# Performance work log

Hardware: AMD Instinct MI355X
Metric: run time of the kernel (lower is better)

The kernel has to match this reference:

```python
import jax, jax.numpy as jnp
import numpy as np

N_C, N_E, IN_FEAT, OUT_FEAT = 8192, 8192, 256, 128


def setup_inputs() -> dict:
    key = jax.random.key(0)
    ks = jax.random.split(key, 9)
    s = 1.0 / np.sqrt(IN_FEAT)
    return {
        "emb_cause": jax.random.normal(ks[0], (N_C, IN_FEAT), jnp.float32),
        "emb_effect": jax.random.normal(ks[1], (N_E, IN_FEAT), jnp.float32),
        "causal_mask": jax.random.randint(ks[2], (N_C, N_E), 0, 2, jnp.int32),
        "Wq": jax.random.uniform(ks[3], (IN_FEAT, OUT_FEAT), jnp.float32, -s, s),
        "bq": jax.random.uniform(ks[4], (OUT_FEAT,), jnp.float32, -s, s),
        "Wk": jax.random.uniform(ks[5], (IN_FEAT, OUT_FEAT), jnp.float32, -s, s),
        "bk": jax.random.uniform(ks[6], (OUT_FEAT,), jnp.float32, -s, s),
        "Wv": jax.random.uniform(ks[7], (IN_FEAT, OUT_FEAT), jnp.float32, -s, s),
        "bv": jax.random.uniform(ks[8], (OUT_FEAT,), jnp.float32, -s, s),
    }


def reference(emb_cause, emb_effect, causal_mask, Wq, bq, Wk, bk, Wv, bv):
    Q = emb_cause @ Wq + bq          # [N_c, D]
    K = emb_effect @ Wk + bk         # [N_e, D]
    V = emb_effect @ Wv + bv         # [N_e, D]
    scale = 1.0 / jnp.sqrt(jnp.asarray(Q.shape[-1], Q.dtype))
    scores = (Q @ K.T) * scale       # [N_c, N_e]
    scores = jnp.where(causal_mask == 0, -jnp.inf, scores)
    attn_weights = jax.nn.softmax(scores, axis=-1)
    causal_output = attn_weights @ V  # [N_c, D]
    return causal_output, attn_weights
```

## Files before the change

### kernel.cpp

```cpp
#include <hip/hip_runtime.h>

#define NC   8192
#define NEFF 8192
#define DIN  256
#define DOUT 128
#define SCALE 0.08838834764831843f

typedef float  f32x4  __attribute__((ext_vector_type(4)));
typedef short  s16x8  __attribute__((ext_vector_type(8)));
typedef short  s16x4  __attribute__((ext_vector_type(4)));
typedef unsigned long long u64;

__device__ __forceinline__ short f2bf(float f) {
    unsigned int u = __builtin_bit_cast(unsigned int, f);
    u += 0x7FFFu + ((u >> 16) & 1u);
    return (short)(u >> 16);
}

__device__ __forceinline__ s16x8 ld8(const short* p) {
    return *(const s16x8*)__builtin_assume_aligned(p, 16);
}

__device__ __forceinline__ unsigned getdw(int4 v, int i) {
    switch (i & 3) {
        case 0: return (unsigned)v.x;
        case 1: return (unsigned)v.y;
        case 2: return (unsigned)v.z;
        default: return (unsigned)v.w;
    }
}


__global__ __launch_bounds__(256) void pack_kernel(
    const int* __restrict__ mask, u64* __restrict__ bm)
{
    const size_t stride = (size_t)gridDim.x * 256;
    const size_t i0 = (size_t)blockIdx.x * 256 + threadIdx.x;
    const bool lead = (threadIdx.x & 63) == 0;
    for (size_t i = i0; i < (size_t)NC * NEFF; i += 8 * stride) {
        int m[8];
#pragma unroll
        for (int j = 0; j < 8; j++) m[j] = mask[i + j * stride];
        u64 b[8];
#pragma unroll
        for (int j = 0; j < 8; j++) b[j] = __ballot(m[j] != 0);
        if (lead) {
#pragma unroll
            for (int j = 0; j < 8; j++) bm[(i + j * stride) >> 6] = b[j];
        }
    }
}

__global__ __launch_bounds__(256, 2) void qkv_kernel(
    const float* __restrict__ embc, const float* __restrict__ embe,
    const float* __restrict__ Wq, const float* __restrict__ bq,
    const float* __restrict__ Wk, const float* __restrict__ bk,
    const float* __restrict__ Wv, const float* __restrict__ bv,
    short* __restrict__ Qf, short* __restrict__ Kf, short* __restrict__ Vf)
{
    const int mat = blockIdx.y;
    const float* src  = (mat == 0) ? embc : embe;
    const float* W    = (mat == 0) ? Wq : (mat == 1 ? Wk : Wv);
    const float* bias = (mat == 0) ? bq : (mat == 1 ? bk : bv);

    __shared__ short wt[DOUT][136];
    __shared__ short tbuf[4][16][132];
    __shared__ short tbufV[128][68];

    const int tid  = threadIdx.x;
    const int wave = tid >> 6, lane = tid & 63;
    const int quad = lane >> 4, ln16 = lane & 15;
    const int rowbase = blockIdx.x * 64;
    const int arow = rowbase + wave * 16 + ln16;

    f32x4 acc[8];
#pragma unroll
    for (int i = 0; i < 8; i++) acc[i] = (f32x4){0.f, 0.f, 0.f, 0.f};

    for (int h = 0; h < 2; h++) {
        __syncthreads();
        {
            const int n0 = (tid & 31) * 4;
            const int kb = tid >> 5;
#pragma unroll
            for (int i = 0; i < 16; i++) {
                const int k = kb + i * 8;
                const float4 w4 = *(const float4*)(W + (size_t)(h * 128 + k) * DOUT + n0);
                wt[n0 + 0][k] = f2bf(w4.x);
                wt[n0 + 1][k] = f2bf(w4.y);
                wt[n0 + 2][k] = f2bf(w4.z);
                wt[n0 + 3][k] = f2bf(w4.w);
            }
        }
        __syncthreads();

        s16x8 afr[4];
#pragma unroll
        for (int kc = 0; kc < 4; kc++) {
            const float* ap = src + (size_t)arow * DIN + h * 128 + kc * 32 + quad * 8;
            const float4 a0 = *(const float4*)ap;
            const float4 a1 = *(const float4*)(ap + 4);
            s16x8 a;
            a[0] = f2bf(a0.x); a[1] = f2bf(a0.y); a[2] = f2bf(a0.z); a[3] = f2bf(a0.w);
            a[4] = f2bf(a1.x); a[5] = f2bf(a1.y); a[6] = f2bf(a1.z); a[7] = f2bf(a1.w);
            afr[kc] = a;
        }
#pragma unroll
        for (int nt = 0; nt < 8; nt++) {
#pragma unroll
            for (int kc = 0; kc < 4; kc++) {
                const s16x8 b = ld8(&wt[nt * 16 + ln16][kc * 32 + quad * 8]);
                acc[nt] = __builtin_amdgcn_mfma_f32_16x16x32_bf16(afr[kc], b, acc[nt], 0, 0, 0);
            }
        }
    }

    if (mat < 2) {
        short* dst = (mat == 0) ? Qf : Kf;
        const float sc = (mat == 0) ? SCALE : 1.0f;
#pragma unroll
        for (int nt = 0; nt < 8; nt++) {
            const float bb = bias[nt * 16 + ln16];
#pragma unroll
            for (int r = 0; r < 4; r++)
                tbuf[wave][quad * 4 + r][nt * 16 + ln16] = f2bf((acc[nt][r] + bb) * sc);
        }
        const int tile = blockIdx.x * 4 + wave;
#pragma unroll
        for (int kc = 0; kc < 4; kc++) {
            const s16x8 fr = ld8(&tbuf[wave][ln16][kc * 32 + quad * 8]);
            *(s16x8*)(dst + ((size_t)(tile * 4 + kc) * 64 + lane) * 8) = fr;
        }
    } else {
#pragma unroll
        for (int nt = 0; nt < 8; nt++) {
            const float bb = bias[nt * 16 + ln16];
#pragma unroll
            for (int r = 0; r < 4; r++)
                tbufV[nt * 16 + ln16][wave * 16 + quad * 4 + r] = f2bf(acc[nt][r] + bb);
        }
        __syncthreads();
        const int ct = blockIdx.x >> 1;
        const int ksub0 = (blockIdx.x & 1) * 2;
        const int ks = wave & 1;
#pragma unroll
        for (int t = 0; t < 4; t++) {
            const int nt2 = (wave >> 1) * 4 + t;
            const s16x8 fr = ld8(&tbufV[nt2 * 16 + ln16][ks * 32 + quad * 8]);
            *(s16x8*)(Vf + ((size_t)((ct * 8 + nt2) * 4 + ksub0 + ks) * 64 + lane) * 8) = fr;
        }
    }
}

__global__ __launch_bounds__(256, 5) void stats_kernel(
    const unsigned int* __restrict__ bm, const short* __restrict__ Qf,
    const short* __restrict__ Kf, float* __restrict__ lsum)
{
    const int bx = blockIdx.x, strip = blockIdx.y;
    const int tid  = threadIdx.x;
    const int wave = tid >> 6, lane = tid & 63;
    const int quad = lane >> 4, ln16 = lane & 15;
    const int rowbase = bx * 128 + wave * 32;
    const int t0 = rowbase >> 4;

    s16x8 aq[2][4];
#pragma unroll
    for (int rs = 0; rs < 2; rs++)
#pragma unroll
        for (int kc = 0; kc < 4; kc++)
            aq[rs][kc] = ld8(Qf + ((size_t)((t0 + rs) * 4 + kc) * 64 + lane) * 8);

    float lp[2] = {0.f, 0.f};

    for (int it = 0; it < 2; it++) {
        const int cb = strip * 256 + it * 128;

        int4 bmv[2];
#pragma unroll
        for (int rs = 0; rs < 2; rs++)
            bmv[rs] = *(const int4*)(bm + (size_t)(rowbase + rs * 16 + ln16) * 256 + (cb >> 5));

#pragma unroll
        for (int nt = 0; nt < 8; nt++) {
            s16x8 bq[4];
#pragma unroll
            for (int kc = 0; kc < 4; kc++)
                bq[kc] = ld8(Kf + ((size_t)(((cb >> 4) + nt) * 4 + kc) * 64 + lane) * 8);
            f32x4 c0 = (f32x4){0.f, 0.f, 0.f, 0.f};
            f32x4 c1 = (f32x4){0.f, 0.f, 0.f, 0.f};
#pragma unroll
            for (int kc = 0; kc < 4; kc++) {
                c0 = __builtin_amdgcn_mfma_f32_16x16x32_bf16(bq[kc], aq[0][kc], c0, 0, 0, 0);
                c1 = __builtin_amdgcn_mfma_f32_16x16x32_bf16(bq[kc], aq[1][kc], c1, 0, 0, 0);
            }
#pragma unroll
            for (int rs = 0; rs < 2; rs++) {
                const unsigned d = getdw(bmv[rs], nt >> 1);
#pragma unroll
                for (int r = 0; r < 4; r++) {
                    const float cv = rs ? c1[r] : c0[r];
                    if ((d >> ((nt & 1) * 16 + quad * 4 + r)) & 1u)
                        lp[rs] += __expf(cv);
                }
            }
        }
    }

#pragma unroll
    for (int rs = 0; rs < 2; rs++) {
        float v = lp[rs];
        v += __shfl_xor(v, 16);
        v += __shfl_xor(v, 32);
        if (quad == 0)
            atomicAdd(&lsum[rowbase + rs * 16 + ln16], v);
    }
}

__global__ __launch_bounds__(256, 3) void attn_kernel(
    const short* __restrict__ Qf, const short* __restrict__ Kf,
    const short* __restrict__ Vf, const float* __restrict__ lsum,
    const unsigned int* __restrict__ bm,
    float* __restrict__ outO, float* __restrict__ outW)
{
    __shared__ short wlds[4][32][132];

    const int bx = blockIdx.x, strip = blockIdx.y;
    const int tid  = threadIdx.x;
    const int wave = tid >> 6, lane = tid & 63;
    const int quad = lane >> 4, ln16 = lane & 15;
    const int rowbase = bx * 128 + wave * 32;
    const int t0 = rowbase >> 4;

    s16x8 aq[2][4];
#pragma unroll
    for (int rs = 0; rs < 2; rs++)
#pragma unroll
        for (int kc = 0; kc < 4; kc++)
            aq[rs][kc] = ld8(Qf + ((size_t)((t0 + rs) * 4 + kc) * 64 + lane) * 8);

    float rl[2];
#pragma unroll
    for (int rs = 0; rs < 2; rs++)
        rl[rs] = 1.0f / lsum[rowbase + rs * 16 + ln16];

    f32x4 o[2][8];
#pragma unroll
    for (int rs = 0; rs < 2; rs++)
#pragma unroll
        for (int i = 0; i < 8; i++) o[rs][i] = (f32x4){0.f, 0.f, 0.f, 0.f};

    for (int it = 0; it < 2; it++) {
        const int cb = strip * 256 + it * 128;

        int4 bmv[2];
#pragma unroll
        for (int rs = 0; rs < 2; rs++)
            bmv[rs] = *(const int4*)(bm + (size_t)(rowbase + rs * 16 + ln16) * 256 + (cb >> 5));

#pragma unroll
        for (int nt = 0; nt < 8; nt++) {
            s16x8 bq[4];
#pragma unroll
            for (int kc = 0; kc < 4; kc++)
                bq[kc] = ld8(Kf + ((size_t)(((cb >> 4) + nt) * 4 + kc) * 64 + lane) * 8);
            f32x4 c0 = (f32x4){0.f, 0.f, 0.f, 0.f};
            f32x4 c1 = (f32x4){0.f, 0.f, 0.f, 0.f};
#pragma unroll
            for (int kc = 0; kc < 4; kc++) {
                c0 = __builtin_amdgcn_mfma_f32_16x16x32_bf16(bq[kc], aq[0][kc], c0, 0, 0, 0);
                c1 = __builtin_amdgcn_mfma_f32_16x16x32_bf16(bq[kc], aq[1][kc], c1, 0, 0, 0);
            }
#pragma unroll
            for (int rs = 0; rs < 2; rs++) {
                const unsigned d = getdw(bmv[rs], nt >> 1);
                float wv[4];
#pragma unroll
                for (int r = 0; r < 4; r++) {
                    const float cv = rs ? c1[r] : c0[r];
                    wv[r] = ((d >> ((nt & 1) * 16 + quad * 4 + r)) & 1u)
                                ? __expf(cv) * rl[rs] : 0.0f;
                }
                const int row = rowbase + rs * 16 + ln16;
                float4 w4; w4.x = wv[0]; w4.y = wv[1]; w4.z = wv[2]; w4.w = wv[3];
                *(float4*)(outW + (size_t)row * NEFF + cb + nt * 16 + quad * 4) = w4;
                s16x4 p4;
                p4[0] = f2bf(wv[0]); p4[1] = f2bf(wv[1]);
                p4[2] = f2bf(wv[2]); p4[3] = f2bf(wv[3]);
                *(s16x4*)__builtin_assume_aligned(
                    &wlds[wave][rs * 16 + ln16][nt * 16 + quad * 4], 8) = p4;
            }
        }

#pragma unroll
        for (int ks = 0; ks < 4; ks++) {
            const s16x8 aw0 = ld8(&wlds[wave][ln16][ks * 32 + quad * 8]);
            const s16x8 aw1 = ld8(&wlds[wave][16 + ln16][ks * 32 + quad * 8]);
#pragma unroll
            for (int nt2 = 0; nt2 < 8; nt2++) {
                const s16x8 bv = ld8(Vf + ((size_t)(((cb >> 7) * 8 + nt2) * 4 + ks) * 64 + lane) * 8);
                o[0][nt2] = __builtin_amdgcn_mfma_f32_16x16x32_bf16(aw0, bv, o[0][nt2], 0, 0, 0);
                o[1][nt2] = __builtin_amdgcn_mfma_f32_16x16x32_bf16(aw1, bv, o[1][nt2], 0, 0, 0);
            }
        }
    }

#pragma unroll
    for (int rs = 0; rs < 2; rs++)
#pragma unroll
        for (int nt2 = 0; nt2 < 8; nt2++)
#pragma unroll
            for (int r = 0; r < 4; r++) {
                const int row = rowbase + rs * 16 + quad * 4 + r;
                atomicAdd(&outO[(size_t)row * DOUT + nt2 * 16 + ln16], o[rs][nt2][r]);
            }
}

extern "C" void kernel_launch(void* const* d_in, const int* in_sizes, int n_in,
                              void* d_out, int out_size, void* d_ws, size_t ws_size,
                              hipStream_t stream) {
    (void)in_sizes; (void)n_in; (void)out_size; (void)ws_size;

    const float* embc = (const float*)d_in[0];
    const float* embe = (const float*)d_in[1];
    const int*   mask = (const int*)d_in[2];
    const float* Wq = (const float*)d_in[3];
    const float* bq = (const float*)d_in[4];
    const float* Wk = (const float*)d_in[5];
    const float* bk = (const float*)d_in[6];
    const float* Wv = (const float*)d_in[7];
    const float* bv = (const float*)d_in[8];

    char* ws = (char*)d_ws;
    short* Qf = (short*)(ws);
    short* Kf = (short*)(ws + (2u << 20));
    short* Vf = (short*)(ws + (4u << 20));
    float* lsum = (float*)(ws + (6u << 20));
    unsigned int* bm = (unsigned int*)(ws + (8u << 20));

    float* outO = (float*)d_out;
    float* outW = outO + (size_t)NC * DOUT;

    hipMemsetAsync(lsum, 0, NC * sizeof(float), stream);
    hipMemsetAsync(outO, 0, (size_t)NC * DOUT * sizeof(float), stream);

    pack_kernel<<<8192, 256, 0, stream>>>(mask, (u64*)bm);
    qkv_kernel<<<dim3(128, 3), 256, 0, stream>>>(embc, embe, Wq, bq, Wk, bk, Wv, bv,
                                                 Qf, Kf, Vf);
    stats_kernel<<<dim3(64, 32), 256, 0, stream>>>(bm, Qf, Kf, lsum);
    attn_kernel<<<dim3(64, 32), 256, 0, stream>>>(Qf, Kf, Vf, lsum, bm, outO, outW);
}
```

Measured before the change: 679.2 us.

## Transpose stats MFMA output layout and halve stats grid with wider strips

The stats kernel now swaps the MFMA operands so each lane holds scores for four rows at one column. The mask bits are then indexed by ln16, and the row sums are reduced across 16 lanes instead of across quads. Each block now covers 512 columns instead of 256, so the grid has half as many strips, fewer atomics are issued, and the loaded Q fragments are reused more. The cost is more registers (8 accumulators and 8 mask vectors), which the occupancy hint lowers from 5 to 4, plus more reduction shuffles.

```diff
diff --git a/kernel.cpp b/kernel.cpp
--- a/kernel.cpp
+++ b/kernel.cpp
@@ -152,7 +152,7 @@
     }
 }
 
-__global__ __launch_bounds__(256, 5) void stats_kernel(
+__global__ __launch_bounds__(256, 4) void stats_kernel(
     const unsigned int* __restrict__ bm, const short* __restrict__ Qf,
     const short* __restrict__ Kf, float* __restrict__ lsum)
 {
@@ -170,15 +170,17 @@
         for (int kc = 0; kc < 4; kc++)
             aq[rs][kc] = ld8(Qf + ((size_t)((t0 + rs) * 4 + kc) * 64 + lane) * 8);
 
-    float lp[2] = {0.f, 0.f};
-
-    for (int it = 0; it < 2; it++) {
-        const int cb = strip * 256 + it * 128;
-
-        int4 bmv[2];
+    float lp[8] = {0.f, 0.f, 0.f, 0.f, 0.f, 0.f, 0.f, 0.f};
+
+    for (int it = 0; it < 4; it++) {
+        const int cb = strip * 512 + it * 128;
+
+        int4 bmv[2][4];
 #pragma unroll
         for (int rs = 0; rs < 2; rs++)
-            bmv[rs] = *(const int4*)(bm + (size_t)(rowbase + rs * 16 + ln16) * 256 + (cb >> 5));
+#pragma unroll
+            for (int r = 0; r < 4; r++)
+                bmv[rs][r] = *(const int4*)(bm + (size_t)(rowbase + rs * 16 + quad * 4 + r) * 256 + (cb >> 5));
 
 #pragma unroll
         for (int nt = 0; nt < 8; nt++) {
@@ -190,29 +192,28 @@
             f32x4 c1 = (f32x4){0.f, 0.f, 0.f, 0.f};
 #pragma unroll
             for (int kc = 0; kc < 4; kc++) {
-                c0 = __builtin_amdgcn_mfma_f32_16x16x32_bf16(bq[kc], aq[0][kc], c0, 0, 0, 0);
-                c1 = __builtin_amdgcn_mfma_f32_16x16x32_bf16(bq[kc], aq[1][kc], c1, 0, 0, 0);
-            }
-#pragma unroll
-            for (int rs = 0; rs < 2; rs++) {
-                const unsigned d = getdw(bmv[rs], nt >> 1);
+                c0 = __builtin_amdgcn_mfma_f32_16x16x32_bf16(aq[0][kc], bq[kc], c0, 0, 0, 0);
+                c1 = __builtin_amdgcn_mfma_f32_16x16x32_bf16(aq[1][kc], bq[kc], c1, 0, 0, 0);
+            }
+#pragma unroll
+            for (int rs = 0; rs < 2; rs++)
 #pragma unroll
                 for (int r = 0; r < 4; r++) {
+                    const unsigned d = getdw(bmv[rs][r], nt >> 1);
                     const float cv = rs ? c1[r] : c0[r];
-                    if ((d >> ((nt & 1) * 16 + quad * 4 + r)) & 1u)
-                        lp[rs] += __expf(cv);
+                    if ((d >> ((nt & 1) * 16 + ln16)) & 1u)
+                        lp[rs * 4 + r] += __expf(cv);
                 }
-            }
-        }
-    }
-
-#pragma unroll
-    for (int rs = 0; rs < 2; rs++) {
-        float v = lp[rs];
-        v += __shfl_xor(v, 16);
-        v += __shfl_xor(v, 32);
-        if (quad == 0)
-            atomicAdd(&lsum[rowbase + rs * 16 + ln16], v);
+        }
+    }
+
+#pragma unroll
+    for (int i = 0; i < 8; i++) {
+        float v = lp[i];
+        v += __shfl_xor(v, 1); v += __shfl_xor(v, 2);
+        v += __shfl_xor(v, 4); v += __shfl_xor(v, 8);
+        if (ln16 == 0)
+            atomicAdd(&lsum[rowbase + (i >> 2) * 16 + quad * 4 + (i & 3)], v);
     }
 }
 
@@ -346,6 +347,6 @@
     pack_kernel<<<8192, 256, 0, stream>>>(mask, (u64*)bm);
     qkv_kernel<<<dim3(128, 3), 256, 0, stream>>>(embc, embe, Wq, bq, Wk, bk, Wv, bv,
                                                  Qf, Kf, Vf);
-    stats_kernel<<<dim3(64, 32), 256, 0, stream>>>(bm, Qf, Kf, lsum);
+    stats_kernel<<<dim3(64, 16), 256, 0, stream>>>(bm, Qf, Kf, lsum);
     attn_kernel<<<dim3(64, 32), 256, 0, stream>>>(Qf, Kf, Vf, lsum, bm, outO, outW);
 }
```

After: 685.6 us. No clear change (+0.9%).

## Retile attention kernel to 16 rows per wave and longer column strips

Applied to the files above, without the earlier changes.

The attention kernel now gives each wave 16 query rows instead of 32 and walks 1024 columns per block instead of 256. The grid changes to 128x8 and launch bounds are raised for occupancy. Fewer strips per row means fewer atomicAdd partial sums into the output. The cost is that each K/V tile loaded is reused by only one row group instead of two, which doubles K and V fetch traffic per MFMA.

```diff
diff --git a/kernel.cpp b/kernel.cpp
--- a/kernel.cpp
+++ b/kernel.cpp
@@ -216,46 +216,37 @@
     }
 }
 
-__global__ __launch_bounds__(256, 3) void attn_kernel(
+__global__ __launch_bounds__(256, 4) void attn_kernel(
     const short* __restrict__ Qf, const short* __restrict__ Kf,
     const short* __restrict__ Vf, const float* __restrict__ lsum,
     const unsigned int* __restrict__ bm,
     float* __restrict__ outO, float* __restrict__ outW)
 {
-    __shared__ short wlds[4][32][132];
+    __shared__ short wlds[4][16][132];
 
     const int bx = blockIdx.x, strip = blockIdx.y;
     const int tid  = threadIdx.x;
     const int wave = tid >> 6, lane = tid & 63;
     const int quad = lane >> 4, ln16 = lane & 15;
-    const int rowbase = bx * 128 + wave * 32;
+    const int rowbase = bx * 64 + wave * 16;
     const int t0 = rowbase >> 4;
 
-    s16x8 aq[2][4];
-#pragma unroll
-    for (int rs = 0; rs < 2; rs++)
-#pragma unroll
-        for (int kc = 0; kc < 4; kc++)
-            aq[rs][kc] = ld8(Qf + ((size_t)((t0 + rs) * 4 + kc) * 64 + lane) * 8);
-
-    float rl[2];
-#pragma unroll
-    for (int rs = 0; rs < 2; rs++)
-        rl[rs] = 1.0f / lsum[rowbase + rs * 16 + ln16];
-
-    f32x4 o[2][8];
-#pragma unroll
-    for (int rs = 0; rs < 2; rs++)
-#pragma unroll
-        for (int i = 0; i < 8; i++) o[rs][i] = (f32x4){0.f, 0.f, 0.f, 0.f};
-
-    for (int it = 0; it < 2; it++) {
-        const int cb = strip * 256 + it * 128;
-
-        int4 bmv[2];
-#pragma unroll
-        for (int rs = 0; rs < 2; rs++)
-            bmv[rs] = *(const int4*)(bm + (size_t)(rowbase + rs * 16 + ln16) * 256 + (cb >> 5));
+    s16x8 aq[4];
+#pragma unroll
+    for (int kc = 0; kc < 4; kc++)
+        aq[kc] = ld8(Qf + ((size_t)(t0 * 4 + kc) * 64 + lane) * 8);
+
+    const int myrow = rowbase + ln16;
+    const float rl = 1.0f / lsum[myrow];
+
+    f32x4 o[8];
+#pragma unroll
+    for (int i = 0; i < 8; i++) o[i] = (f32x4){0.f, 0.f, 0.f, 0.f};
+
+    for (int it = 0; it < 8; it++) {
+        const int cb = strip * 1024 + it * 128;
+
+        const int4 bmv = *(const int4*)(bm + (size_t)myrow * 256 + (cb >> 5));
 
 #pragma unroll
         for (int nt = 0; nt < 8; nt++) {
@@ -263,56 +254,44 @@
 #pragma unroll
             for (int kc = 0; kc < 4; kc++)
                 bq[kc] = ld8(Kf + ((size_t)(((cb >> 4) + nt) * 4 + kc) * 64 + lane) * 8);
-            f32x4 c0 = (f32x4){0.f, 0.f, 0.f, 0.f};
-            f32x4 c1 = (f32x4){0.f, 0.f, 0.f, 0.f};
-#pragma unroll
-            for (int kc = 0; kc < 4; kc++) {
-                c0 = __builtin_amdgcn_mfma_f32_16x16x32_bf16(bq[kc], aq[0][kc], c0, 0, 0, 0);
-                c1 = __builtin_amdgcn_mfma_f32_16x16x32_bf16(bq[kc], aq[1][kc], c1, 0, 0, 0);
-            }
-#pragma unroll
-            for (int rs = 0; rs < 2; rs++) {
-                const unsigned d = getdw(bmv[rs], nt >> 1);
-                float wv[4];
-#pragma unroll
-                for (int r = 0; r < 4; r++) {
-                    const float cv = rs ? c1[r] : c0[r];
-                    wv[r] = ((d >> ((nt & 1) * 16 + quad * 4 + r)) & 1u)
-                                ? __expf(cv) * rl[rs] : 0.0f;
-                }
-                const int row = rowbase + rs * 16 + ln16;
-                float4 w4; w4.x = wv[0]; w4.y = wv[1]; w4.z = wv[2]; w4.w = wv[3];
-                *(float4*)(outW + (size_t)row * NEFF + cb + nt * 16 + quad * 4) = w4;
-                s16x4 p4;
-                p4[0] = f2bf(wv[0]); p4[1] = f2bf(wv[1]);
-                p4[2] = f2bf(wv[2]); p4[3] = f2bf(wv[3]);
-                *(s16x4*)__builtin_assume_aligned(
-                    &wlds[wave][rs * 16 + ln16][nt * 16 + quad * 4], 8) = p4;
-            }
+            f32x4 c = (f32x4){0.f, 0.f, 0.f, 0.f};
+#pragma unroll
+            for (int kc = 0; kc < 4; kc++)
+                c = __builtin_amdgcn_mfma_f32_16x16x32_bf16(bq[kc], aq[kc], c, 0, 0, 0);
+            const unsigned d = getdw(bmv, nt >> 1);
+            float wv[4];
+#pragma unroll
+            for (int r = 0; r < 4; r++) {
+                wv[r] = ((d >> ((nt & 1) * 16 + quad * 4 + r)) & 1u)
+                            ? __expf(c[r]) * rl : 0.0f;
+            }
+            float4 w4; w4.x = wv[0]; w4.y = wv[1]; w4.z = wv[2]; w4.w = wv[3];
+            *(float4*)(outW + (size_t)myrow * NEFF + cb + nt * 16 + quad * 4) = w4;
+            s16x4 p4;
+            p4[0] = f2bf(wv[0]); p4[1] = f2bf(wv[1]);
+            p4[2] = f2bf(wv[2]); p4[3] = f2bf(wv[3]);
+            *(s16x4*)__builtin_assume_aligned(
+                &wlds[wave][ln16][nt * 16 + quad * 4], 8) = p4;
         }
 
 #pragma unroll
         for (int ks = 0; ks < 4; ks++) {
-            const s16x8 aw0 = ld8(&wlds[wave][ln16][ks * 32 + quad * 8]);
-            const s16x8 aw1 = ld8(&wlds[wave][16 + ln16][ks * 32 + quad * 8]);
+            const s16x8 aw = ld8(&wlds[wave][ln16][ks * 32 + quad * 8]);
 #pragma unroll
             for (int nt2 = 0; nt2 < 8; nt2++) {
                 const s16x8 bv = ld8(Vf + ((size_t)(((cb >> 7) * 8 + nt2) * 4 + ks) * 64 + lane) * 8);
-                o[0][nt2] = __builtin_amdgcn_mfma_f32_16x16x32_bf16(aw0, bv, o[0][nt2], 0, 0, 0);
-                o[1][nt2] = __builtin_amdgcn_mfma_f32_16x16x32_bf16(aw1, bv, o[1][nt2], 0, 0, 0);
-            }
-        }
-    }
-
-#pragma unroll
-    for (int rs = 0; rs < 2; rs++)
-#pragma unroll
-        for (int nt2 = 0; nt2 < 8; nt2++)
-#pragma unroll
-            for (int r = 0; r < 4; r++) {
-                const int row = rowbase + rs * 16 + quad * 4 + r;
-                atomicAdd(&outO[(size_t)row * DOUT + nt2 * 16 + ln16], o[rs][nt2][r]);
-            }
+                o[nt2] = __builtin_amdgcn_mfma_f32_16x16x32_bf16(aw, bv, o[nt2], 0, 0, 0);
+            }
+        }
+    }
+
+#pragma unroll
+    for (int nt2 = 0; nt2 < 8; nt2++)
+#pragma unroll
+        for (int r = 0; r < 4; r++) {
+            const int row = rowbase + quad * 4 + r;
+            atomicAdd(&outO[(size_t)row * DOUT + nt2 * 16 + ln16], o[nt2][r]);
+        }
 }
 
 extern "C" void kernel_launch(void* const* d_in, const int* in_sizes, int n_in,
@@ -347,5 +326,5 @@
     qkv_kernel<<<dim3(128, 3), 256, 0, stream>>>(embc, embe, Wq, bq, Wk, bk, Wv, bv,
                                                  Qf, Kf, Vf);
     stats_kernel<<<dim3(64, 32), 256, 0, stream>>>(bm, Qf, Kf, lsum);
-    attn_kernel<<<dim3(64, 32), 256, 0, stream>>>(Qf, Kf, Vf, lsum, bm, outO, outW);
-}
+    attn_kernel<<<dim3(128, 8), 256, 0, stream>>>(Qf, Kf, Vf, lsum, bm, outO, outW);
+}
```

Result: no change. 674.1 us (-0.7%).
